# Kernel tuning notes

Hardware: AMD Instinct MI355X
Metric: run time of the kernel (lower is better)

## Reference

```python
import jax, jax.numpy as jnp
import numpy as np


def setup_inputs() -> dict:
    key = jax.random.key(0)
    kx, kw = jax.random.split(key)
    x = jax.random.normal(kx, (8192, 4096), dtype=jnp.float32)
    # weights initialized ~ N(0, 0.1) as in RandomNormal(stddev=0.1)
    w = jax.random.normal(kw, (4096, 4096), dtype=jnp.float32) * 0.1
    return {"x": x, "w": w}


def reference(x, w):
    # BinaryDense: sign-binarize both activations and weights, then matmul.
    x_bin = jnp.sign(x)  # [N, d_in], values in {-1, 0, +1}
    w_bin = jnp.sign(w)  # [d_in, units]
    return jnp.matmul(x_bin, w_bin)  # [N, units]
```

## Files before the change

kernel.cpp:

```cpp
#include <hip/hip_runtime.h>


#define M_DIM 8192
#define K_DIM 4096
#define N_DIM 4096
#define KB2   (K_DIM / 2)
#define NK    (K_DIM / 128)
#define BUFB  (128 * 64)

typedef int   v4i  __attribute__((ext_vector_type(4)));
typedef int   v8i  __attribute__((ext_vector_type(8)));
typedef float v16f __attribute__((ext_vector_type(16)));

__device__ __forceinline__ unsigned int nib4(float x) {
    return x > 0.0f ? 0x2u : (x < 0.0f ? 0xAu : 0x0u);
}

__global__ __launch_bounds__(256) void pack_both(const float* __restrict__ x,
                                                 unsigned short* __restrict__ xq,
                                                 const float* __restrict__ w,
                                                 unsigned char* __restrict__ wT) {
    if (blockIdx.x < 32768u) {
        size_t t = (size_t)blockIdx.x * 256 + threadIdx.x;
        float4 f = ((const float4*)x)[t];
        unsigned int v = nib4(f.x) | (nib4(f.y) << 4) | (nib4(f.z) << 8) | (nib4(f.w) << 12);
        xq[t] = (unsigned short)v;
        return;
    }
    __shared__ unsigned char sT[64][132];
    const unsigned id = blockIdx.x - 32768u;
    const int t  = threadIdx.x;
    const int n0 = (int)(id & 31) * 128;
    const int kb = (int)(id >> 5);
    const int k0 = kb * 64;

    const int cq = t & 31;
    const int r0 = t >> 5;
#pragma unroll
    for (int p = 0; p < 8; ++p) {
        int r = r0 + 8 * p;
        float4 f = *(const float4*)(w + (size_t)(k0 + r) * N_DIM + n0 + cq * 4);
        uchar4 c;
        c.x = (unsigned char)nib4(f.x);
        c.y = (unsigned char)nib4(f.y);
        c.z = (unsigned char)nib4(f.z);
        c.w = (unsigned char)nib4(f.w);
        *(uchar4*)(&sT[r][cq * 4]) = c;
    }
    __syncthreads();

    const int n  = t >> 1;
    const int kq = t & 1;
    union { unsigned char b[16]; int4 v; } u;
#pragma unroll
    for (int j = 0; j < 16; ++j) {
        unsigned lo = sT[kq * 32 + 2 * j][n];
        unsigned hi = sT[kq * 32 + 2 * j + 1][n];
        u.b[j] = (unsigned char)(lo | (hi << 4));
    }
    *(int4*)(wT + (size_t)(n0 + n) * KB2 + (size_t)kb * 32 + kq * 16) = u.v;
}

__device__ __forceinline__ v8i widen(v4i x) {
    v8i r;
    r[0] = x[0]; r[1] = x[1]; r[2] = x[2]; r[3] = x[3];
    r[4] = 0; r[5] = 0; r[6] = 0; r[7] = 0;
    return r;
}

__global__ __launch_bounds__(256) void bgemm_fp4(const unsigned char* __restrict__ A,
                                                 const unsigned char* __restrict__ B,
                                                 float* __restrict__ C) {
    __shared__ unsigned char sA[2 * BUFB];
    __shared__ unsigned char sB[2 * BUFB];

    const int tid  = threadIdx.x;
    const int lane = tid & 63;
    const int wave = tid >> 6;
    const int wm   = wave >> 1;
    const int wn   = wave & 1;
    const int l31  = lane & 31;
    const int lhi  = lane >> 5;

    const int m0 = blockIdx.y * 128;
    const int n0 = blockIdx.x * 128;

    v16f acc[2][2] = {};

    const unsigned char* gA[2];
    const unsigned char* gB[2];
    int ldsOff[2];
#pragma unroll
    for (int i = 0; i < 2; ++i) {
        int g  = tid + i * 256;
        int m  = g >> 2;
        int kc = (g & 3) ^ ((m >> 1) & 3);
        gA[i] = A + (size_t)(m0 + m) * KB2 + kc * 16;
        gB[i] = B + (size_t)(n0 + m) * KB2 + kc * 16;
        ldsOff[i] = g * 16;
    }

    int offA[2][2], offB[2][2];
#pragma unroll
    for (int ks = 0; ks < 2; ++ks) {
#pragma unroll
        for (int tmn = 0; tmn < 2; ++tmn) {
            int mloc = wm * 64 + tmn * 32 + l31;
            int nloc = wn * 64 + tmn * 32 + l31;
            int kcm  = (ks * 2 + lhi) ^ ((mloc >> 1) & 3);
            int kcn  = (ks * 2 + lhi) ^ ((nloc >> 1) & 3);
            offA[ks][tmn] = mloc * 64 + kcm * 16;
            offB[ks][tmn] = nloc * 64 + kcn * 16;
        }
    }

    auto compute = [&](int bo) {
#pragma unroll
        for (int ks = 0; ks < 2; ++ks) {
            v4i a4[2], b4[2];
#pragma unroll
            for (int tm = 0; tm < 2; ++tm) a4[tm] = *(const v4i*)(sA + bo + offA[ks][tm]);
#pragma unroll
            for (int tn = 0; tn < 2; ++tn) b4[tn] = *(const v4i*)(sB + bo + offB[ks][tn]);
#pragma unroll
            for (int tm = 0; tm < 2; ++tm)
#pragma unroll
                for (int tn = 0; tn < 2; ++tn)
                    acc[tm][tn] = __builtin_amdgcn_mfma_scale_f32_32x32x64_f8f6f4(
                        widen(a4[tm]), widen(b4[tn]), acc[tm][tn],
                        4, 4,
                        0, 0x7F7F7F7F,
                        0, 0x7F7F7F7F);
        }
    };

    v4i rA[2], rB[2];
#pragma unroll
    for (int i = 0; i < 2; ++i) { rA[i] = *(const v4i*)gA[i]; rB[i] = *(const v4i*)gB[i]; }
#pragma unroll
    for (int i = 0; i < 2; ++i) {
        *(v4i*)(sA + ldsOff[i]) = rA[i];
        *(v4i*)(sB + ldsOff[i]) = rB[i];
    }
    __syncthreads();

    for (int kt = 0; kt < NK - 1; ++kt) {
        const size_t koff = (size_t)(kt + 1) * 64;
#pragma unroll
        for (int i = 0; i < 2; ++i) {
            rA[i] = *(const v4i*)(gA[i] + koff);
            rB[i] = *(const v4i*)(gB[i] + koff);
        }
        compute((kt & 1) * BUFB);
        const int bn = ((kt + 1) & 1) * BUFB;
#pragma unroll
        for (int i = 0; i < 2; ++i) {
            *(v4i*)(sA + bn + ldsOff[i]) = rA[i];
            *(v4i*)(sB + bn + ldsOff[i]) = rB[i];
        }
        __syncthreads();
    }
    compute(((NK - 1) & 1) * BUFB);

#pragma unroll
    for (int tm = 0; tm < 2; ++tm) {
#pragma unroll
        for (int tn = 0; tn < 2; ++tn) {
            const int col  = n0 + wn * 64 + tn * 32 + l31;
            const int rowb = m0 + wm * 64 + tm * 32 + 4 * lhi;
#pragma unroll
            for (int r = 0; r < 16; ++r) {
                int row = rowb + (r & 3) + 8 * (r >> 2);
                __builtin_nontemporal_store(acc[tm][tn][r], &C[(size_t)row * N_DIM + col]);
            }
        }
    }
}

extern "C" void kernel_launch(void* const* d_in, const int* in_sizes, int n_in,
                              void* d_out, int out_size, void* d_ws, size_t ws_size,
                              hipStream_t stream) {
    const float* x = (const float*)d_in[0];
    const float* w = (const float*)d_in[1];
    float* out = (float*)d_out;

    unsigned char* xq = (unsigned char*)d_ws;
    unsigned char* wq = xq + (size_t)M_DIM * KB2;

    pack_both<<<dim3(32768 + 2048), dim3(256), 0, stream>>>(
        x, (unsigned short*)xq, w, wq);
    bgemm_fp4<<<dim3(N_DIM / 128, M_DIM / 128), dim3(256), 0, stream>>>(xq, wq, out);
}
```

Baseline: 324.8 us.

## Enlarge FP4 GEMM tiles to 256x256 with async global-to-LDS loads

```diff
diff --git a/kernel.cpp b/kernel.cpp
--- a/kernel.cpp
+++ b/kernel.cpp
@@ -5,8 +5,10 @@
 #define K_DIM 4096
 #define N_DIM 4096
 #define KB2   (K_DIM / 2)
-#define NK    (K_DIM / 128)
-#define BUFB  (128 * 64)
+#define BKB   128
+#define NKT   (KB2 / BKB)
+#define TILEB (256 * BKB)
+#define BUFB  (2 * TILEB)
 
 typedef int   v4i  __attribute__((ext_vector_type(4)));
 typedef int   v8i  __attribute__((ext_vector_type(8)));
@@ -68,62 +70,82 @@
     return r;
 }
 
-__global__ __launch_bounds__(256) void bgemm_fp4(const unsigned char* __restrict__ A,
-                                                 const unsigned char* __restrict__ B,
-                                                 float* __restrict__ C) {
-    __shared__ unsigned char sA[2 * BUFB];
-    __shared__ unsigned char sB[2 * BUFB];
+__device__ __forceinline__ void gload16(const unsigned char* g, unsigned char* l) {
+    __builtin_amdgcn_global_load_lds(
+        (__attribute__((address_space(1))) void*)(void*)g,
+        (__attribute__((address_space(3))) void*)l, 16, 0, 0);
+}
+
+__global__ __launch_bounds__(512, 2) void bgemm_fp4(const unsigned char* __restrict__ A,
+                                                    const unsigned char* __restrict__ B,
+                                                    float* __restrict__ C) {
+    __shared__ __align__(16) unsigned char lds[2 * BUFB];
 
     const int tid  = threadIdx.x;
     const int lane = tid & 63;
     const int wave = tid >> 6;
-    const int wm   = wave >> 1;
-    const int wn   = wave & 1;
+    const int wm   = wave >> 2;
+    const int wn   = wave & 3;
     const int l31  = lane & 31;
     const int lhi  = lane >> 5;
 
-    const int m0 = blockIdx.y * 128;
-    const int n0 = blockIdx.x * 128;
+    const int m0 = blockIdx.y * 256;
+    const int n0 = blockIdx.x * 256;
 
-    v16f acc[2][2] = {};
+    v16f acc[4][2] = {};
 
-    const unsigned char* gA[2];
-    const unsigned char* gB[2];
-    int ldsOff[2];
+    const unsigned char* gA[4];
+    const unsigned char* gB[4];
+    int dstOff[4];
 #pragma unroll
-    for (int i = 0; i < 2; ++i) {
-        int g  = tid + i * 256;
-        int m  = g >> 2;
-        int kc = (g & 3) ^ ((m >> 1) & 3);
-        gA[i] = A + (size_t)(m0 + m) * KB2 + kc * 16;
-        gB[i] = B + (size_t)(n0 + m) * KB2 + kc * 16;
-        ldsOff[i] = g * 16;
+    for (int i = 0; i < 4; ++i) {
+        int g   = i * 512 + tid;
+        int row = g >> 3;
+        int kc  = (g & 7) ^ (row & 7);
+        gA[i] = A + (size_t)(m0 + row) * KB2 + kc * 16;
+        gB[i] = B + (size_t)(n0 + row) * KB2 + kc * 16;
+        dstOff[i] = g * 16;
     }
 
-    int offA[2][2], offB[2][2];
+    int offA[4][4], offB[4][2];
 #pragma unroll
-    for (int ks = 0; ks < 2; ++ks) {
+    for (int ks = 0; ks < 4; ++ks) {
 #pragma unroll
-        for (int tmn = 0; tmn < 2; ++tmn) {
-            int mloc = wm * 64 + tmn * 32 + l31;
-            int nloc = wn * 64 + tmn * 32 + l31;
-            int kcm  = (ks * 2 + lhi) ^ ((mloc >> 1) & 3);
-            int kcn  = (ks * 2 + lhi) ^ ((nloc >> 1) & 3);
-            offA[ks][tmn] = mloc * 64 + kcm * 16;
-            offB[ks][tmn] = nloc * 64 + kcn * 16;
+        for (int tm = 0; tm < 4; ++tm) {
+            int r  = wm * 128 + tm * 32 + l31;
+            int kc = (2 * ks + lhi) ^ (r & 7);
+            offA[ks][tm] = r * BKB + kc * 16;
+        }
+#pragma unroll
+        for (int tn = 0; tn < 2; ++tn) {
+            int r  = wn * 64 + tn * 32 + l31;
+            int kc = (2 * ks + lhi) ^ (r & 7);
+            offB[ks][tn] = r * BKB + kc * 16;
         }
     }
 
-    auto compute = [&](int bo) {
+    auto stage = [&](int kt, int b) {
+        unsigned char* s = lds + b * BUFB;
+        const size_t ko = (size_t)kt * BKB;
 #pragma unroll
-        for (int ks = 0; ks < 2; ++ks) {
-            v4i a4[2], b4[2];
+        for (int i = 0; i < 4; ++i) {
+            gload16(gA[i] + ko, s + dstOff[i]);
+            gload16(gB[i] + ko, s + TILEB + dstOff[i]);
+        }
+    };
+
+    auto compute = [&](int b) {
+        const unsigned char* sA = lds + b * BUFB;
+        const unsigned char* sB = sA + TILEB;
 #pragma unroll
-            for (int tm = 0; tm < 2; ++tm) a4[tm] = *(const v4i*)(sA + bo + offA[ks][tm]);
+        for (int ks = 0; ks < 4; ++ks) {
+            v4i a4[4], b4[2];
 #pragma unroll
-            for (int tn = 0; tn < 2; ++tn) b4[tn] = *(const v4i*)(sB + bo + offB[ks][tn]);
+            for (int tm = 0; tm < 4; ++tm) a4[tm] = *(const v4i*)(sA + offA[ks][tm]);
 #pragma unroll
-            for (int tm = 0; tm < 2; ++tm)
+            for (int tn = 0; tn < 2; ++tn) b4[tn] = *(const v4i*)(sB + offB[ks][tn]);
+#pragma unroll
+            for (int tm = 0; tm < 4; ++tm)
 #pragma unroll
                 for (int tn = 0; tn < 2; ++tn)
                     acc[tm][tn] = __builtin_amdgcn_mfma_scale_f32_32x32x64_f8f6f4(
@@ -134,40 +156,19 @@
         }
     };
 
-    v4i rA[2], rB[2];
-#pragma unroll
-    for (int i = 0; i < 2; ++i) { rA[i] = *(const v4i*)gA[i]; rB[i] = *(const v4i*)gB[i]; }
-#pragma unroll
-    for (int i = 0; i < 2; ++i) {
-        *(v4i*)(sA + ldsOff[i]) = rA[i];
-        *(v4i*)(sB + ldsOff[i]) = rB[i];
+    stage(0, 0);
+    for (int kt = 0; kt < NKT; ++kt) {
+        __syncthreads();
+        if (kt + 1 < NKT) stage(kt + 1, (kt + 1) & 1);
+        compute(kt & 1);
     }
-    __syncthreads();
-
-    for (int kt = 0; kt < NK - 1; ++kt) {
-        const size_t koff = (size_t)(kt + 1) * 64;
-#pragma unroll
-        for (int i = 0; i < 2; ++i) {
-            rA[i] = *(const v4i*)(gA[i] + koff);
-            rB[i] = *(const v4i*)(gB[i] + koff);
-        }
-        compute((kt & 1) * BUFB);
-        const int bn = ((kt + 1) & 1) * BUFB;
-#pragma unroll
-        for (int i = 0; i < 2; ++i) {
-            *(v4i*)(sA + bn + ldsOff[i]) = rA[i];
-            *(v4i*)(sB + bn + ldsOff[i]) = rB[i];
-        }
-        __syncthreads();
-    }
-    compute(((NK - 1) & 1) * BUFB);
 
 #pragma unroll
-    for (int tm = 0; tm < 2; ++tm) {
+    for (int tm = 0; tm < 4; ++tm) {
 #pragma unroll
         for (int tn = 0; tn < 2; ++tn) {
             const int col  = n0 + wn * 64 + tn * 32 + l31;
-            const int rowb = m0 + wm * 64 + tm * 32 + 4 * lhi;
+            const int rowb = m0 + wm * 128 + tm * 32 + 4 * lhi;
 #pragma unroll
             for (int r = 0; r < 16; ++r) {
                 int row = rowb + (r & 3) + 8 * (r >> 2);
@@ -189,5 +190,5 @@
 
     pack_both<<<dim3(32768 + 2048), dim3(256), 0, stream>>>(
         x, (unsigned short*)xq, w, wq);
-    bgemm_fp4<<<dim3(N_DIM / 128, M_DIM / 128), dim3(256), 0, stream>>>(xq, wq, out);
+    bgemm_fp4<<<dim3(N_DIM / 256, M_DIM / 256), dim3(512), 0, stream>>>(xq, wq, out);
 }
```

Measured after the change: 321.6 us. About the same (-1.0%).
